# Performance work log

Measured on AMD Instinct MI355X. Metric: run time of the kernel, lower is better.

The kernel has to match this reference:

```python
import jax, jax.numpy as jnp
import numpy as np

EPS = 1e-5
P, B, T, C = 2, 8, 1024, 1024
H = 4 * C

def layernorm(x, g, b):
    mu = jnp.mean(x, axis=-1, keepdims=True)
    var = jnp.var(x, axis=-1, keepdims=True)
    return (x - mu) * jax.lax.rsqrt(var + EPS) * g + b

def time_shift(x):
    # ZeroPad2d((0,0,1,-1)): xx[t] = x[t-1], xx[0] = 0 along the T axis
    pad = [(0, 0)] * (x.ndim - 2) + [(1, 0), (0, 0)]
    return jnp.pad(x, pad)[..., :-1, :]

def wkv(time_decay, time_first, k, v):
    # Faithful port of the RWKV-v4 CUDA WKV scan (numerically stable form).
    # k, v: [N, T, C]; time_decay/time_first: [C]
    w = -jnp.exp(time_decay)  # decay (negative)
    u = time_first
    kT = jnp.moveaxis(k, 1, 0)  # [T, N, C]
    vT = jnp.moveaxis(v, 1, 0)
    N = k.shape[0]
    Cc = k.shape[2]

    def step(carry, kv):
        aa, bb, pp = carry
        kk, vv = kv
        ww = u + kk
        p = jnp.maximum(pp, ww)
        e1 = jnp.exp(pp - p)
        e2 = jnp.exp(ww - p)
        y = (e1 * aa + e2 * vv) / (e1 * bb + e2)
        ww2 = w + pp
        p2 = jnp.maximum(ww2, kk)
        e1b = jnp.exp(ww2 - p2)
        e2b = jnp.exp(kk - p2)
        return (e1b * aa + e2b * vv, e1b * bb + e2b, p2), y

    init = (jnp.zeros((N, Cc), jnp.float32), jnp.zeros((N, Cc), jnp.float32),
            jnp.full((N, Cc), -1e38, jnp.float32))
    _, yT = jax.lax.scan(step, init, (kT, vT))
    return jnp.moveaxis(yT, 0, 1)  # [N, T, C]


def setup_inputs() -> dict:
    key = jax.random.key(0)
    ks = jax.random.split(key, 20)
    f32 = jnp.float32
    layer_id, n_layer = 1, 12
    ratio_0_to_1 = layer_id / (n_layer - 1)
    ratio_1_to_almost0 = 1.0 - layer_id / n_layer
    xcurve = (np.arange(C, dtype=np.float32) / C).reshape(1, 1, C)
    decay_speed = -5 + 8 * (np.arange(C, dtype=np.float32) / (C - 1)) ** (0.7 + 1.3 * ratio_0_to_1)
    zigzag = (np.array([(i + 1) % 3 - 1 for i in range(C)], dtype=np.float32)) * 0.5
    time_first = np.ones(C, dtype=np.float32) * np.log(0.3) + zigzag
    mk = np.stack([xcurve ** ratio_1_to_almost0 for _ in range(P)], 0)  # [P,1,1,C]
    mv = np.stack([xcurve ** ratio_1_to_almost0 + 0.3 * ratio_0_to_1 for _ in range(P)], 0)
    mr = np.stack([xcurve ** (0.5 * ratio_1_to_almost0) for _ in range(P)], 0)
    s = 0.02
    return {
        'x': jax.random.normal(ks[0], (P, B, T, C), f32),
        'ln1_g': jnp.ones((C,), f32), 'ln1_b': jnp.zeros((C,), f32),
        'ln2_g': jnp.ones((C,), f32), 'ln2_b': jnp.zeros((C,), f32),
        'time_decay': jnp.asarray(decay_speed, f32),
        'time_first': jnp.asarray(time_first, f32),
        'att_mix_k': jnp.asarray(mk, f32), 'att_mix_v': jnp.asarray(mv, f32),
        'att_mix_r': jnp.asarray(mr, f32),
        'Wk': jax.random.normal(ks[1], (C, C), f32) * s,
        'Wv': jax.random.normal(ks[2], (C, C), f32) * s,
        'Wr': jax.random.normal(ks[3], (C, C), f32) * s,
        'Wo': jax.random.normal(ks[4], (C, C), f32) * s,
        'cm_mix_k': jnp.asarray(mk, f32), 'cm_mix_r': jnp.asarray(mk, f32),
        'Wck': jax.random.normal(ks[5], (H, C), f32) * s,
        'Wcr': jax.random.normal(ks[6], (C, C), f32) * s,
        'Wcv': jax.random.normal(ks[7], (C, H), f32) * s,
    }


def reference(x, ln1_g, ln1_b, ln2_g, ln2_b, time_decay, time_first,
              att_mix_k, att_mix_v, att_mix_r, Wk, Wv, Wr, Wo,
              cm_mix_k, cm_mix_r, Wck, Wcr, Wcv):
    p, b, t, c = x.shape
    # --- TimeMix branch: x = x + Wo @ (sigmoid(r) * WKV(k, v)) ---
    h = layernorm(x, ln1_g, ln1_b)
    xx = time_shift(h)
    xk = h * att_mix_k + xx * (1 - att_mix_k)
    xv = h * att_mix_v + xx * (1 - att_mix_v)
    xr = h * att_mix_r + xx * (1 - att_mix_r)
    k = jnp.einsum('pbtc,dc->pbtd', xk, Wk)
    v = jnp.einsum('pbtc,dc->pbtd', xv, Wv)
    sr = jax.nn.sigmoid(jnp.einsum('pbtc,dc->pbtd', xr, Wr))
    y = wkv(time_decay, time_first,
            k.reshape(p * b, t, c), v.reshape(p * b, t, c)).reshape(p, b, t, c)
    x = x + jnp.einsum('pbtc,dc->pbtd', sr * y, Wo)
    # --- ChannelMix branch ---
    h = layernorm(x, ln2_g, ln2_b)
    xx = time_shift(h)
    xk = h * cm_mix_k + xx * (1 - cm_mix_k)
    xr = h * cm_mix_r + xx * (1 - cm_mix_r)
    kk = jnp.einsum('pbtc,hc->pbth', xk, Wck)
    kk = jnp.square(jax.nn.relu(kk))
    kv = jnp.einsum('pbth,ch->pbtc', kk, Wcv)
    out = jax.nn.sigmoid(jnp.einsum('pbtc,dc->pbtd', xr, Wcr)) * kv
    return x + out
```

## Files before the change

### kernel.cpp

```cpp
#include <hip/hip_runtime.h>

#define T_SEQ 1024
#define C_DIM 1024
#define H_DIM 4096
#define M_ROWS 16384
#define CHUNKS 16
#define CLEN 64

typedef _Float16 f16x8 __attribute__((ext_vector_type(8)));
typedef _Float16 f16x4 __attribute__((ext_vector_type(4)));
typedef float    f32x4 __attribute__((ext_vector_type(4)));

#define AS1 __attribute__((address_space(1)))
#define AS3 __attribute__((address_space(3)))

__device__ __forceinline__ void gload_lds16(const void* g, void* l) {
  __builtin_amdgcn_global_load_lds((const AS1 void*)g, (AS3 void*)l, 16, 0, 0);
}

__device__ __forceinline__ float sigmoidf_(float x) {
  return 1.0f / (1.0f + __expf(-x));
}

struct CvtArgs {
  const float* src[7];
  _Float16*    dst[7];
  int n4[7];
  int start[8];
};

__global__ __launch_bounds__(256) void cvt_all_kernel(CvtArgs a) {
  const int bid = blockIdx.x;
  int s = 0;
#pragma unroll
  for (int j = 0; j < 7; ++j) s += (bid >= a.start[j + 1]) ? 1 : 0;
  const int i = (bid - a.start[s]) * 256 + threadIdx.x;
  if (i >= a.n4[s]) return;
  f32x4 v = reinterpret_cast<const f32x4*>(a.src[s])[i];
  f16x4 o;
  o[0] = (_Float16)v[0]; o[1] = (_Float16)v[1];
  o[2] = (_Float16)v[2]; o[3] = (_Float16)v[3];
  reinterpret_cast<f16x4*>(a.dst[s])[i] = o;
}

__global__ __launch_bounds__(256) void ln_kernel(const float* __restrict__ x,
    const float* __restrict__ g, const float* __restrict__ b,
    _Float16* __restrict__ h) {
  const int row  = blockIdx.x * 4 + (threadIdx.x >> 6);
  const int lane = threadIdx.x & 63;
  const f32x4* xr = reinterpret_cast<const f32x4*>(x + (size_t)row * C_DIM);
  f32x4 v[4];
  float s = 0.f, sq = 0.f;
#pragma unroll
  for (int i = 0; i < 4; ++i) {
    v[i] = xr[i * 64 + lane];
#pragma unroll
    for (int j = 0; j < 4; ++j) { s += v[i][j]; sq += v[i][j] * v[i][j]; }
  }
#pragma unroll
  for (int off = 32; off > 0; off >>= 1) {
    s  += __shfl_xor(s, off, 64);
    sq += __shfl_xor(sq, off, 64);
  }
  const float mu   = s * (1.0f / C_DIM);
  const float var  = sq * (1.0f / C_DIM) - mu * mu;
  const float rstd = rsqrtf(var + 1e-5f);
  const f32x4* g4 = reinterpret_cast<const f32x4*>(g);
  const f32x4* b4 = reinterpret_cast<const f32x4*>(b);
  f16x4* h4 = reinterpret_cast<f16x4*>(h + (size_t)row * C_DIM);
#pragma unroll
  for (int i = 0; i < 4; ++i) {
    f32x4 gg = g4[i * 64 + lane];
    f32x4 bb = b4[i * 64 + lane];
    f16x4 o;
#pragma unroll
    for (int j = 0; j < 4; ++j)
      o[j] = (_Float16)((v[i][j] - mu) * rstd * gg[j] + bb[j]);
    h4[i * 64 + lane] = o;
  }
}

__global__ __launch_bounds__(256) void mix3_kernel(const _Float16* __restrict__ h,
    const float* __restrict__ mk, const float* __restrict__ mv, const float* __restrict__ mr,
    _Float16* __restrict__ xk, _Float16* __restrict__ xv, _Float16* __restrict__ xr) {
  const int i  = blockIdx.x * 256 + threadIdx.x;
  const int m  = i >> 7;
  const int c0 = (i & 127) << 3;
  const int p  = m >> 13;
  const int t  = m & (T_SEQ - 1);
  const f16x8* h8 = reinterpret_cast<const f16x8*>(h);
  f16x8 hc = h8[i];
  f16x8 hp;
#pragma unroll
  for (int j = 0; j < 8; ++j) hp[j] = (_Float16)0.f;
  if (t) hp = h8[i - 128];
  f16x8 ok, ov, orr;
#pragma unroll
  for (int j = 0; j < 8; ++j) {
    const float hcf = (float)hc[j], hpf = (float)hp[j];
    const float a = mk[p * C_DIM + c0 + j];
    const float c = mv[p * C_DIM + c0 + j];
    const float d = mr[p * C_DIM + c0 + j];
    ok[j]  = (_Float16)(hcf * a + hpf * (1.f - a));
    ov[j]  = (_Float16)(hcf * c + hpf * (1.f - c));
    orr[j] = (_Float16)(hcf * d + hpf * (1.f - d));
  }
  reinterpret_cast<f16x8*>(xk)[i] = ok;
  reinterpret_cast<f16x8*>(xv)[i] = ov;
  reinterpret_cast<f16x8*>(xr)[i] = orr;
}

__global__ __launch_bounds__(256) void mix2_kernel(const _Float16* __restrict__ h,
    const float* __restrict__ mk, const float* __restrict__ mr,
    _Float16* __restrict__ xk, _Float16* __restrict__ xr) {
  const int i  = blockIdx.x * 256 + threadIdx.x;
  const int m  = i >> 7;
  const int c0 = (i & 127) << 3;
  const int p  = m >> 13;
  const int t  = m & (T_SEQ - 1);
  const f16x8* h8 = reinterpret_cast<const f16x8*>(h);
  f16x8 hc = h8[i];
  f16x8 hp;
#pragma unroll
  for (int j = 0; j < 8; ++j) hp[j] = (_Float16)0.f;
  if (t) hp = h8[i - 128];
  f16x8 ok, orr;
#pragma unroll
  for (int j = 0; j < 8; ++j) {
    const float hcf = (float)hc[j], hpf = (float)hp[j];
    const float a = mk[p * C_DIM + c0 + j];
    const float d = mr[p * C_DIM + c0 + j];
    ok[j]  = (_Float16)(hcf * a + hpf * (1.f - a));
    orr[j] = (_Float16)(hcf * d + hpf * (1.f - d));
  }
  reinterpret_cast<f16x8*>(xk)[i] = ok;
  reinterpret_cast<f16x8*>(xr)[i] = orr;
}

__global__ __launch_bounds__(1024, 1) void wkv_kernel(const _Float16* __restrict__ k,
    const _Float16* __restrict__ v, const _Float16* __restrict__ r,
    const float* __restrict__ td, const float* __restrict__ tf,
    _Float16* __restrict__ a_out) {
  __shared__ float sA[CHUNKS][64];
  __shared__ float sB[CHUNKS][64];
  __shared__ float sP[CHUNKS][64];
  const int tid   = threadIdx.x;
  const int chunk = tid >> 6;
  const int ch    = tid & 63;
  const int n     = blockIdx.x >> 4;
  const int cg    = blockIdx.x & 15;
  const int c     = cg * 64 + ch;
  const float w = -__expf(td[c]);
  const float u = tf[c];
  const size_t cbase = (size_t)n * T_SEQ * C_DIM + (size_t)chunk * CLEN * C_DIM + c;

  float aa = 0.f, bb = 0.f, pp = -1e38f;
  for (int s = 0; s < CLEN; ++s) {
    const size_t idx = cbase + (size_t)s * C_DIM;
    const float kk = (float)k[idx];
    const float vv = (float)v[idx];
    const float ww2 = w + pp;
    const float p2  = fmaxf(ww2, kk);
    const float e1b = __expf(ww2 - p2);
    const float e2b = __expf(kk - p2);
    aa = e1b * aa + e2b * vv;
    bb = e1b * bb + e2b;
    pp = p2;
  }
  sA[chunk][ch] = aa; sB[chunk][ch] = bb; sP[chunk][ch] = pp;
  __syncthreads();

  if (chunk == 0) {
    float pa = 0.f, pb = 0.f, ppr = -1e38f;
    const float wL = w * (float)CLEN;
    for (int j = 0; j < CHUNKS; ++j) {
      const float la = sA[j][ch], lb = sB[j][ch], lp = sP[j][ch];
      sA[j][ch] = pa; sB[j][ch] = pb; sP[j][ch] = ppr;
      const float dp = wL + ppr;
      const float np = fmaxf(dp, lp);
      const float e1 = __expf(dp - np);
      const float e2 = __expf(lp - np);
      pa  = e1 * pa + e2 * la;
      pb  = e1 * pb + e2 * lb;
      ppr = np;
    }
  }
  __syncthreads();

  aa = sA[chunk][ch]; bb = sB[chunk][ch]; pp = sP[chunk][ch];
  for (int s = 0; s < CLEN; ++s) {
    const size_t idx = cbase + (size_t)s * C_DIM;
    const float kk = (float)k[idx];
    const float vv = (float)v[idx];
    const float ww = u + kk;
    const float p  = fmaxf(pp, ww);
    const float e1 = __expf(pp - p);
    const float e2 = __expf(ww - p);
    const float yv = __fdividef(e1 * aa + e2 * vv, e1 * bb + e2);
    const float sr = sigmoidf_((float)r[idx]);
    a_out[idx] = (_Float16)(sr * yv);
    const float ww2 = w + pp;
    const float p2  = fmaxf(ww2, kk);
    const float e1b = __expf(ww2 - p2);
    const float e2b = __expf(kk - p2);
    aa = e1b * aa + e2b * vv;
    bb = e1b * bb + e2b;
    pp = p2;
  }
}

#define GBAR() do { __builtin_amdgcn_sched_barrier(0); \
                    __builtin_amdgcn_s_barrier(); \
                    __builtin_amdgcn_sched_barrier(0); } while (0)
#define WVN(n) do { asm volatile("s_waitcnt vmcnt(" #n ")" ::: "memory"); \
                    __builtin_amdgcn_sched_barrier(0); } while (0)
#define WLN(n) do { asm volatile("s_waitcnt lgkmcnt(" #n ")" ::: "memory"); \
                    __builtin_amdgcn_sched_barrier(0); } while (0)
#define STAGE(op, SRC, row0, k0, bb) do { \
    _Pragma("unroll") \
    for (int c_ = 0; c_ < 2; ++c_) { \
      gload_lds16((SRC) + (size_t)((row0) + c_ * 64) * K + (k0), \
                  &lds[bb][op][((size_t)((row0) + c_ * 64) << 6) + dbase]); \
    } } while (0)
#define RD_AH(dst, mh) do { \
    _Pragma("unroll") for (int i_ = 0; i_ < 4; ++i_) \
    _Pragma("unroll") for (int k_ = 0; k_ < 2; ++k_) \
      dst[i_][k_] = *reinterpret_cast<const f16x8*>( \
        &lds[bi][0][((wr * 128 + (mh) * 64 + i_ * 16 + frow) << 6) + \
                    (((k_ << 5) + fk) ^ fxorh)]); \
  } while (0)
#define RD_BH(dst, nh) do { \
    _Pragma("unroll") for (int j_ = 0; j_ < 2; ++j_) \
    _Pragma("unroll") for (int k_ = 0; k_ < 2; ++k_) \
      dst[j_][k_] = *reinterpret_cast<const f16x8*>( \
        &lds[bi][1][((wcn * 64 + (nh) * 32 + j_ * 16 + frow) << 6) + \
                    (((k_ << 5) + fk) ^ fxorh)]); \
  } while (0)
#define MM16(asrc, bsrc, mh, nh) do { \
    __builtin_amdgcn_s_setprio(1); \
    _Pragma("unroll") for (int k_ = 0; k_ < 2; ++k_) \
    _Pragma("unroll") for (int i_ = 0; i_ < 4; ++i_) \
    _Pragma("unroll") for (int j_ = 0; j_ < 2; ++j_) \
      acc[(mh) * 4 + i_][(nh) * 2 + j_] = __builtin_amdgcn_mfma_f32_16x16x32_f16( \
        asrc[i_][k_], bsrc[j_][k_], acc[(mh) * 4 + i_][(nh) * 2 + j_], 0, 0, 0); \
    __builtin_amdgcn_s_setprio(0); \
  } while (0)

template<int EPI>
__global__ __launch_bounds__(512, 2) void gemm_nt_256(
    const _Float16* __restrict__ A, const _Float16* __restrict__ B,
    void* __restrict__ Cv, const float* __restrict__ X,
    const _Float16* __restrict__ KV, int M, int N, int K) {
  __shared__ _Float16 lds[2][2][256 * 64];
  const int tid  = threadIdx.x;
  const int wave = tid >> 6;
  const int lane = tid & 63;
  const int wr   = wave >> 2;
  const int wcn  = wave & 3;

  const unsigned nwx  = gridDim.x;
  const unsigned pery = gridDim.y >> 3;
  const unsigned id   = blockIdx.y * nwx + blockIdx.x;
  const unsigned xcd  = id & 7;
  const unsigned loc  = id >> 3;
  const size_t m0 = (size_t)(xcd * pery + loc / nwx) * 256;
  const size_t n0 = (size_t)(loc % nwx) * 256;

  const int srow  = tid >> 3;
  const int scolh = ((tid & 7) ^ (srow & 7)) << 3;
  const size_t dbase = (size_t)(srow & ~7) << 6;
  const _Float16* sA = A + (m0 + srow) * (size_t)K + scolh;
  const _Float16* sB = B + (n0 + srow) * (size_t)K + scolh;

  const int frow  = lane & 15;
  const int fk    = (lane >> 4) << 3;
  const int fxorh = (frow & 7) << 3;

  f32x4 acc[8][4];
#pragma unroll
  for (int i = 0; i < 8; ++i)
#pragma unroll
    for (int j = 0; j < 4; ++j) acc[i][j] = (f32x4){0.f, 0.f, 0.f, 0.f};

  STAGE(0, sA, 0, 0, 0); STAGE(0, sA, 128, 0, 0);
  STAGE(1, sB, 0, 0, 0); STAGE(1, sB, 128, 0, 0);

  const int NT = K >> 6;
  for (int t = 0; t < NT; ++t) {
    const int bi = t & 1;
    const int nb = bi ^ 1;
    const int k1 = (t + 1) << 6;
    const bool st = (t + 1) < NT;
    f16x8 af[4][2], b0f[2][2], b1f[2][2];
    if (st) { STAGE(0, sA, 0, k1, nb); WVN(2); }
    else    { WVN(0); }
    GBAR();
    RD_AH(af, 0); RD_BH(b0f, 0);
    WLN(0);
    MM16(af, b0f, 0, 0);
    GBAR();
    RD_BH(b1f, 1);
    if (st) STAGE(1, sB, 0, k1, nb);
    GBAR();
    WLN(0);
    MM16(af, b1f, 0, 1);
    GBAR();
    RD_AH(af, 1);
    if (st) STAGE(1, sB, 128, k1, nb);
    GBAR();
    WLN(0);
    MM16(af, b0f, 1, 0);
    GBAR();
    if (st) STAGE(0, sA, 128, k1, nb);
    GBAR();
    WLN(0);
    MM16(af, b1f, 1, 1);
    GBAR();
  }

  const int ecol  = lane & 15;
  const int erow4 = (lane >> 4) * 4;
#pragma unroll
  for (int mf = 0; mf < 8; ++mf)
#pragma unroll
    for (int nf = 0; nf < 4; ++nf) {
      const size_t rbase = m0 + (size_t)(wr * 128 + mf * 16 + erow4);
      const size_t cc    = n0 + (size_t)(wcn * 64 + nf * 16 + ecol);
#pragma unroll
      for (int r = 0; r < 4; ++r) {
        const float val = acc[mf][nf][r];
        const size_t off = (rbase + r) * (size_t)N + cc;
        if constexpr (EPI == 0) {
          ((_Float16*)Cv)[off] = (_Float16)val;
        } else if constexpr (EPI == 1) {
          const float tq = fmaxf(val, 0.f);
          ((_Float16*)Cv)[off] = (_Float16)(tq * tq);
        } else if constexpr (EPI == 2) {
          ((float*)Cv)[off] = val + X[off];
        } else {
          ((float*)Cv)[off] = X[off] + sigmoidf_(val) * (float)KV[off];
        }
      }
    }
}

extern "C" void kernel_launch(void* const* d_in, const int* in_sizes, int n_in,
                              void* d_out, int out_size, void* d_ws, size_t ws_size,
                              hipStream_t stream) {
  const float* x      = (const float*)d_in[0];
  const float* ln1_g  = (const float*)d_in[1];
  const float* ln1_b  = (const float*)d_in[2];
  const float* ln2_g  = (const float*)d_in[3];
  const float* ln2_b  = (const float*)d_in[4];
  const float* tdec   = (const float*)d_in[5];
  const float* tfirst = (const float*)d_in[6];
  const float* amk    = (const float*)d_in[7];
  const float* amv    = (const float*)d_in[8];
  const float* amr    = (const float*)d_in[9];
  const float* Wk     = (const float*)d_in[10];
  const float* Wv     = (const float*)d_in[11];
  const float* Wr     = (const float*)d_in[12];
  const float* Wo     = (const float*)d_in[13];
  const float* cmk    = (const float*)d_in[14];
  const float* cmr    = (const float*)d_in[15];
  const float* Wck    = (const float*)d_in[16];
  const float* Wcr    = (const float*)d_in[17];
  const float* Wcv    = (const float*)d_in[18];

  char* ws = (char*)d_ws;
  const size_t SZ = (size_t)M_ROWS * C_DIM * sizeof(_Float16);
  _Float16* B0 = (_Float16*)(ws + 0 * SZ);
  _Float16* B1 = (_Float16*)(ws + 1 * SZ);
  _Float16* B2 = (_Float16*)(ws + 2 * SZ);
  _Float16* B3 = (_Float16*)(ws + 3 * SZ);
  _Float16* B4 = (_Float16*)(ws + 4 * SZ);
  _Float16* B5 = (_Float16*)(ws + 5 * SZ);
  _Float16* B6 = (_Float16*)(ws + 6 * SZ);
  _Float16* wWk  = (_Float16*)(ws + 7 * SZ);
  _Float16* wWv  = wWk  + (size_t)C_DIM * C_DIM;
  _Float16* wWr  = wWv  + (size_t)C_DIM * C_DIM;
  _Float16* wWo  = wWr  + (size_t)C_DIM * C_DIM;
  _Float16* wWcr = wWo  + (size_t)C_DIM * C_DIM;
  _Float16* wWck = wWcr + (size_t)C_DIM * C_DIM;
  _Float16* wWcv = wWck + (size_t)H_DIM * C_DIM;

  {
    CvtArgs a;
    const float* srcs[7] = {Wk, Wv, Wr, Wo, Wcr, Wck, Wcv};
    _Float16*    dsts[7] = {wWk, wWv, wWr, wWo, wWcr, wWck, wWcv};
    const size_t ns[7]   = {(size_t)C_DIM * C_DIM, (size_t)C_DIM * C_DIM,
                            (size_t)C_DIM * C_DIM, (size_t)C_DIM * C_DIM,
                            (size_t)C_DIM * C_DIM, (size_t)H_DIM * C_DIM,
                            (size_t)C_DIM * H_DIM};
    int st = 0;
    for (int j = 0; j < 7; ++j) {
      a.src[j] = srcs[j]; a.dst[j] = dsts[j];
      a.n4[j] = (int)(ns[j] / 4);
      a.start[j] = st;
      st += (a.n4[j] + 255) / 256;
    }
    a.start[7] = st;
    cvt_all_kernel<<<dim3(st), dim3(256), 0, stream>>>(a);
  }

  const dim3 blk(256);
  const dim3 gblk(512);
  const dim3 gN1(C_DIM / 256, M_ROWS / 256);
  const dim3 gN4(H_DIM / 256, M_ROWS / 256);

  ln_kernel<<<dim3(M_ROWS / 4), blk, 0, stream>>>(x, ln1_g, ln1_b, B0);
  mix3_kernel<<<dim3(M_ROWS * 128 / 256), blk, 0, stream>>>(B0, amk, amv, amr, B1, B2, B3);
  gemm_nt_256<0><<<gN1, gblk, 0, stream>>>(B1, wWk, B4, nullptr, nullptr, M_ROWS, C_DIM, C_DIM);
  gemm_nt_256<0><<<gN1, gblk, 0, stream>>>(B2, wWv, B5, nullptr, nullptr, M_ROWS, C_DIM, C_DIM);
  gemm_nt_256<0><<<gN1, gblk, 0, stream>>>(B3, wWr, B6, nullptr, nullptr, M_ROWS, C_DIM, C_DIM);
  wkv_kernel<<<dim3(256), dim3(1024), 0, stream>>>(B4, B5, B6, tdec, tfirst, B1);
  gemm_nt_256<2><<<gN1, gblk, 0, stream>>>(B1, wWo, d_out, x, nullptr, M_ROWS, C_DIM, C_DIM);

  ln_kernel<<<dim3(M_ROWS / 4), blk, 0, stream>>>((const float*)d_out, ln2_g, ln2_b, B0);
  mix2_kernel<<<dim3(M_ROWS * 128 / 256), blk, 0, stream>>>(B0, cmk, cmr, B1, B2);
  gemm_nt_256<1><<<gN4, gblk, 0, stream>>>(B1, wWck, B3, nullptr, nullptr, M_ROWS, H_DIM, C_DIM);
  gemm_nt_256<0><<<gN1, gblk, 0, stream>>>(B3, wWcv, B1, nullptr, nullptr, M_ROWS, C_DIM, H_DIM);
  gemm_nt_256<3><<<gN1, gblk, 0, stream>>>(B2, wWcr, d_out, (const float*)d_out, B1,
                                           M_ROWS, C_DIM, C_DIM);
}
```

Measured before the change: 659.0 us.

## Batch K/V/R GEMMs via grid z and prefetch GEMM tiles two stages ahead

The three TimeMix projection GEMMs are merged into a single launch, with blockIdx.z selecting per-batch offsets for A, B and C through new stride arguments. This aims to cut launch overhead and fill more CUs than a 256-block grid can. The GEMM main loop is also restructured so the first A and B half-tiles of iteration t+2 are issued one iteration earlier, with adjusted vmcnt waits, to hide global-to-LDS latency better. Batching relies on the activation, weight and output buffers for k/v/r being laid out contiguously at the given strides.

```diff
diff --git a/kernel.cpp b/kernel.cpp
--- a/kernel.cpp
+++ b/kernel.cpp
@@ -216,6 +216,7 @@
                     __builtin_amdgcn_sched_barrier(0); } while (0)
 #define WLN(n) do { asm volatile("s_waitcnt lgkmcnt(" #n ")" ::: "memory"); \
                     __builtin_amdgcn_sched_barrier(0); } while (0)
+#define SCHED() __builtin_amdgcn_sched_barrier(0)
 #define STAGE(op, SRC, row0, k0, bb) do { \
     _Pragma("unroll") \
     for (int c_ = 0; c_ < 2; ++c_) { \
@@ -250,13 +251,18 @@
 __global__ __launch_bounds__(512, 2) void gemm_nt_256(
     const _Float16* __restrict__ A, const _Float16* __restrict__ B,
     void* __restrict__ Cv, const float* __restrict__ X,
-    const _Float16* __restrict__ KV, int M, int N, int K) {
+    const _Float16* __restrict__ KV, int M, int N, int K,
+    size_t strideA, size_t strideB, size_t strideCbytes) {
   __shared__ _Float16 lds[2][2][256 * 64];
   const int tid  = threadIdx.x;
   const int wave = tid >> 6;
   const int lane = tid & 63;
   const int wr   = wave >> 2;
   const int wcn  = wave & 3;
+
+  A  = A + (size_t)blockIdx.z * strideA;
+  B  = B + (size_t)blockIdx.z * strideB;
+  Cv = (void*)((char*)Cv + (size_t)blockIdx.z * strideCbytes);
 
   const unsigned nwx  = gridDim.x;
   const unsigned pery = gridDim.y >> 3;
@@ -282,39 +288,56 @@
 #pragma unroll
     for (int j = 0; j < 4; ++j) acc[i][j] = (f32x4){0.f, 0.f, 0.f, 0.f};
 
-  STAGE(0, sA, 0, 0, 0); STAGE(0, sA, 128, 0, 0);
-  STAGE(1, sB, 0, 0, 0); STAGE(1, sB, 128, 0, 0);
-
   const int NT = K >> 6;
+  STAGE(0, sA, 0,   0, 0);
+  STAGE(1, sB, 0,   0, 0);
+  STAGE(1, sB, 128, 0, 0);
+  STAGE(0, sA, 128, 0, 0);
+  if (NT > 1) {
+    STAGE(0, sA, 0, 64, 1);
+    STAGE(1, sB, 0, 64, 1);
+    WVN(4);
+  } else {
+    WVN(0);
+  }
+  GBAR();
+
   for (int t = 0; t < NT; ++t) {
     const int bi = t & 1;
     const int nb = bi ^ 1;
     const int k1 = (t + 1) << 6;
-    const bool st = (t + 1) < NT;
-    f16x8 af[4][2], b0f[2][2], b1f[2][2];
-    if (st) { STAGE(0, sA, 0, k1, nb); WVN(2); }
-    else    { WVN(0); }
-    GBAR();
-    RD_AH(af, 0); RD_BH(b0f, 0);
+    const int k2 = (t + 2) << 6;
+    const bool s1 = (t + 1) < NT;
+    const bool s2 = (t + 2) < NT;
+    f16x8 a0[4][2], a1[4][2], b0[2][2], b1[2][2];
+    RD_AH(a0, 0); RD_BH(b0, 0); SCHED();
+    if (s1) STAGE(1, sB, 128, k1, nb);
+    WLN(8);
+    GBAR();
     WLN(0);
-    MM16(af, b0f, 0, 0);
-    GBAR();
-    RD_BH(b1f, 1);
-    if (st) STAGE(1, sB, 0, k1, nb);
+    MM16(a0, b0, 0, 0);
+    GBAR();
+    RD_BH(b1, 1); SCHED();
+    if (s1) STAGE(0, sA, 128, k1, nb);
     GBAR();
     WLN(0);
-    MM16(af, b1f, 0, 1);
-    GBAR();
-    RD_AH(af, 1);
-    if (st) STAGE(1, sB, 128, k1, nb);
+    MM16(a0, b1, 0, 1);
+    GBAR();
+    RD_AH(a1, 1); SCHED();
+    if (s2) STAGE(0, sA, 0, k2, bi);
     GBAR();
     WLN(0);
-    MM16(af, b0f, 1, 0);
-    GBAR();
-    if (st) STAGE(0, sA, 128, k1, nb);
+    MM16(a1, b0, 1, 0);
+    GBAR();
+    if (s2) {
+      STAGE(1, sB, 0, k2, bi);
+      WVN(4);
+    } else {
+      WVN(0);
+    }
     GBAR();
     WLN(0);
-    MM16(af, b1f, 1, 1);
+    MM16(a1, b1, 1, 1);
     GBAR();
   }
 
@@ -406,20 +429,25 @@
   const dim3 blk(256);
   const dim3 gblk(512);
   const dim3 gN1(C_DIM / 256, M_ROWS / 256);
+  const dim3 gKVR(C_DIM / 256, M_ROWS / 256, 3);
   const dim3 gN4(H_DIM / 256, M_ROWS / 256);
 
   ln_kernel<<<dim3(M_ROWS / 4), blk, 0, stream>>>(x, ln1_g, ln1_b, B0);
   mix3_kernel<<<dim3(M_ROWS * 128 / 256), blk, 0, stream>>>(B0, amk, amv, amr, B1, B2, B3);
-  gemm_nt_256<0><<<gN1, gblk, 0, stream>>>(B1, wWk, B4, nullptr, nullptr, M_ROWS, C_DIM, C_DIM);
-  gemm_nt_256<0><<<gN1, gblk, 0, stream>>>(B2, wWv, B5, nullptr, nullptr, M_ROWS, C_DIM, C_DIM);
-  gemm_nt_256<0><<<gN1, gblk, 0, stream>>>(B3, wWr, B6, nullptr, nullptr, M_ROWS, C_DIM, C_DIM);
+  gemm_nt_256<0><<<gKVR, gblk, 0, stream>>>(B1, wWk, B4, nullptr, nullptr,
+      M_ROWS, C_DIM, C_DIM,
+      (size_t)M_ROWS * C_DIM, (size_t)C_DIM * C_DIM,
+      (size_t)M_ROWS * C_DIM * sizeof(_Float16));
   wkv_kernel<<<dim3(256), dim3(1024), 0, stream>>>(B4, B5, B6, tdec, tfirst, B1);
-  gemm_nt_256<2><<<gN1, gblk, 0, stream>>>(B1, wWo, d_out, x, nullptr, M_ROWS, C_DIM, C_DIM);
+  gemm_nt_256<2><<<gN1, gblk, 0, stream>>>(B1, wWo, d_out, x, nullptr,
+      M_ROWS, C_DIM, C_DIM, 0, 0, 0);
 
   ln_kernel<<<dim3(M_ROWS / 4), blk, 0, stream>>>((const float*)d_out, ln2_g, ln2_b, B0);
   mix2_kernel<<<dim3(M_ROWS * 128 / 256), blk, 0, stream>>>(B0, cmk, cmr, B1, B2);
-  gemm_nt_256<1><<<gN4, gblk, 0, stream>>>(B1, wWck, B3, nullptr, nullptr, M_ROWS, H_DIM, C_DIM);
-  gemm_nt_256<0><<<gN1, gblk, 0, stream>>>(B3, wWcv, B1, nullptr, nullptr, M_ROWS, C_DIM, H_DIM);
+  gemm_nt_256<1><<<gN4, gblk, 0, stream>>>(B1, wWck, B3, nullptr, nullptr,
+      M_ROWS, H_DIM, C_DIM, 0, 0, 0);
+  gemm_nt_256<0><<<gN1, gblk, 0, stream>>>(B3, wWcv, B1, nullptr, nullptr,
+      M_ROWS, C_DIM, H_DIM, 0, 0, 0);
   gemm_nt_256<3><<<gN1, gblk, 0, stream>>>(B2, wWcr, d_out, (const float*)d_out, B1,
-                                           M_ROWS, C_DIM, C_DIM);
-}
+      M_ROWS, C_DIM, C_DIM, 0, 0, 0);
+}
```

Result: faster. 636.5 us (-3.4%).
